# Kernel tuning notes

Measured on AMD Instinct MI355X. Metric: run time of the kernel, lower is better.

The kernel has to match this reference:

```python
import jax, jax.numpy as jnp
import numpy as np
from jax import lax

D_MODEL = 512
N_STATE = 64
L = 1024
NC = 4  # n_components
HIDDEN = 2 * D_MODEL  # ChannelMix mult=2
R = D_MODEL // 8      # SE reduction
EPS = 1e-5


def hippo_A(N):
    n = np.arange(N, dtype=np.float32)
    t = 2.0 * n + 1.0
    sq = np.sqrt(t[:, None] * t[None, :])
    A = -np.tril(sq, -1) - np.diag(n + 1.0)
    return jnp.asarray(A, jnp.float32)


def setup_inputs() -> dict:
    key = jax.random.key(0)
    ks = jax.random.split(key, 12)
    d, N = D_MODEL, N_STATE
    n = np.arange(N, dtype=np.float32)
    Bref = jnp.asarray(np.sqrt(2.0 * n + 1.0), jnp.float32)
    Bp = jnp.tile(Bref[None, None, :], (NC, d, 1)) + 0.01 * jax.random.normal(ks[0], (NC, d, N))
    Cp = 0.1 * jax.random.normal(ks[1], (NC, d, N))
    Dp = jnp.zeros((NC, d))
    log_dt = jnp.log(0.1 * (1.5 ** jnp.arange(NC, dtype=jnp.float32)))
    x = jax.random.normal(ks[2], (8, L, d))
    s = 0.02
    return {
        "x": x,
        "Bp": Bp, "Cp": Cp, "Dp": Dp, "log_dt": log_dt,
        "se_w1": s * jax.random.normal(ks[3], (R, d)), "se_b1": jnp.zeros((R,)),
        "se_w2": s * jax.random.normal(ks[4], (d, R)), "se_b2": jnp.zeros((d,)),
        "n1_g": jnp.ones((d,)), "n1_b": jnp.zeros((d,)),
        "up_w": s * jax.random.normal(ks[5], (2 * HIDDEN, d)), "up_b": jnp.zeros((2 * HIDDEN,)),
        "down_w": s * jax.random.normal(ks[6], (d, HIDDEN)), "down_b": jnp.zeros((d,)),
        "mixn_g": jnp.ones((d,)), "mixn_b": jnp.zeros((d,)),
        "n2_g": jnp.ones((d,)), "n2_b": jnp.zeros((d,)),
    }


def _ln(x, g, b):
    m = jnp.mean(x, axis=-1, keepdims=True)
    v = jnp.mean(jnp.square(x - m), axis=-1, keepdims=True)
    return (x - m) * lax.rsqrt(v + EPS) * g + b


def _mixture_kernel(Bp, Cp, Dp, log_dt):
    A = hippo_A(N_STATE)
    I = jnp.eye(N_STATE, dtype=jnp.float32)

    def one(Bc, Cc, Dc, ldt):
        dt = jax.nn.softplus(ldt) + 1e-6
        lhs = I - 0.5 * dt * A
        rhs = I + 0.5 * dt * A
        A_bar = jnp.linalg.solve(lhs, rhs)          # (N,N)
        B_bar = jnp.linalg.solve(lhs, (dt * Bc).T).T  # (d,N)

        def step(xs, _):
            y = jnp.einsum('dn,dn->d', Cc, xs)
            return xs @ A_bar.T, y

        _, ys = lax.scan(step, B_bar, None, length=L)  # (L,d)
        K = ys.T  # (d,L)
        return K.at[:, 0].add(Dc)

    return jax.vmap(one)(Bp, Cp, Dp, log_dt).sum(0)  # (d,L)


def reference(x, Bp, Cp, Dp, log_dt,
              se_w1, se_b1, se_w2, se_b2,
              n1_g, n1_b, up_w, up_b, down_w, down_b,
              mixn_g, mixn_b, n2_g, n2_b):
    d = D_MODEL
    K = _mixture_kernel(Bp, Cp, Dp, log_dt)  # (d,L)

    # causal full-length depthwise conv1d
    x_dw = jnp.transpose(x, (0, 2, 1))  # (B,C,T)
    x_pad = jnp.pad(x_dw, ((0, 0), (0, 0), (L - 1, 0)))
    y = lax.conv_general_dilated(
        x_pad, K[:, None, :], window_strides=(1,), padding='VALID',
        feature_group_count=d, dimension_numbers=('NCH', 'OIH', 'NCH'))
    y = jnp.transpose(y, (0, 2, 1))  # (B,T,C)

    # SE gate (squeeze over time)
    s = jnp.mean(y, axis=1)  # (B,C)
    h = jax.nn.relu(s @ se_w1.T + se_b1)
    g = jax.nn.sigmoid(h @ se_w2.T + se_b2)
    y = y * g[:, None, :]

    y1 = _ln(x + y, n1_g, n1_b)

    # ChannelMix (GLU MLP) with residual + LN
    u = y1 @ up_w.T + up_b
    a, gg = jnp.split(u, 2, axis=-1)
    z = (jax.nn.gelu(a, approximate=False) * jax.nn.sigmoid(gg)) @ down_w.T + down_b
    z = _ln(y1 + z, mixn_g, mixn_b)

    return _ln(y1 + z, n2_g, n2_b)
```

## Files before the change

kernel.cpp:

```cpp
#include <hip/hip_runtime.h>
#include <math.h>


typedef short bf16x8 __attribute__((ext_vector_type(8)));
typedef float f32x4 __attribute__((ext_vector_type(4)));

__device__ __forceinline__ float sigmoidf_(float x) { return 1.0f / (1.0f + expf(-x)); }
__device__ __forceinline__ float geluf_(float x) { return 0.5f * x * (1.0f + erff(x * 0.70710678118654752f)); }
__device__ __forceinline__ unsigned short f2bf(float f) {
    unsigned u = __float_as_uint(f);
    unsigned r = (u + 0x7FFFu + ((u >> 16) & 1u)) >> 16;
    return (unsigned short)r;
}
__device__ __forceinline__ unsigned pk2(unsigned short a, unsigned short b) {
    return (unsigned)a | ((unsigned)b << 16);
}

__global__ __launch_bounds__(256) void prep_comp(const float* __restrict__ log_dt,
                                                 float* __restrict__ Pow,
                                                 float* __restrict__ dtbuf) {
    int comp = blockIdx.x, tid = threadIdx.x;
    __shared__ __align__(16) float M1[4096];
    __shared__ __align__(16) float M1T[4096];
    __shared__ __align__(16) float M2[4096];
    __shared__ __align__(16) float M2T[4096];
    float ldt = log_dt[comp];
    float dt = log1pf(expf(ldt)) + 1e-6f;
    float hdt = 0.5f * dt;
    if (tid < 64) {
        int j = tid;
        float sqj = sqrtf(2.0f * (float)j + 1.0f);
        float S = 0.0f;
        for (int i = 0; i < 64; ++i) {
            float sqi = sqrtf(2.0f * (float)i + 1.0f);
            float r = (i == j) ? (1.0f - hdt * (float)(i + 1))
                               : ((i > j) ? (-hdt * sqi * sqj) : 0.0f);
            float X = (r - hdt * sqi * S) / (1.0f + hdt * (float)(i + 1));
            M1[i * 64 + j] = X;
            M1T[j * 64 + i] = X;
            S += sqi * X;
        }
    }
    __syncthreads();
    for (int ii = tid; ii < 4096; ii += 256) Pow[(size_t)comp * 40960 + ii] = M1[ii];
    float* cur = M1; float* curT = M1T; float* nxt = M2; float* nxtT = M2T;
    int ti = tid >> 4, tj = tid & 15;
    for (int s = 1; s <= 9; ++s) {
        float c[4][4] = {{0}};
#pragma unroll 8
        for (int k = 0; k < 64; ++k) {
            float4 a = *(const float4*)&curT[k * 64 + ti * 4];
            float4 b = *(const float4*)&cur[k * 64 + tj * 4];
            c[0][0] += a.x * b.x; c[0][1] += a.x * b.y; c[0][2] += a.x * b.z; c[0][3] += a.x * b.w;
            c[1][0] += a.y * b.x; c[1][1] += a.y * b.y; c[1][2] += a.y * b.z; c[1][3] += a.y * b.w;
            c[2][0] += a.z * b.x; c[2][1] += a.z * b.y; c[2][2] += a.z * b.z; c[2][3] += a.z * b.w;
            c[3][0] += a.w * b.x; c[3][1] += a.w * b.y; c[3][2] += a.w * b.z; c[3][3] += a.w * b.w;
        }
#pragma unroll
        for (int r = 0; r < 4; ++r) {
            float4 row; row.x = c[r][0]; row.y = c[r][1]; row.z = c[r][2]; row.w = c[r][3];
            *(float4*)&nxt[(ti * 4 + r) * 64 + tj * 4] = row;
            float4 colv; colv.x = c[0][r]; colv.y = c[1][r]; colv.z = c[2][r]; colv.w = c[3][r];
            *(float4*)&nxtT[(tj * 4 + r) * 64 + ti * 4] = colv;
        }
        __syncthreads();
        for (int ii = tid; ii < 4096; ii += 256) Pow[(size_t)comp * 40960 + s * 4096 + ii] = nxt[ii];
        float* t0 = cur; cur = nxt; nxt = t0;
        float* t1 = curT; curT = nxtT; nxtT = t1;
        __syncthreads();
    }
    if (tid == 0) dtbuf[comp] = dt;
}

__global__ __launch_bounds__(256) void compute_bbar(const float* __restrict__ Bp,
                                                    const float* __restrict__ dtbuf,
                                                    float* __restrict__ Bbar) {
    int gid = blockIdx.x * 256 + threadIdx.x;
    int comp = gid >> 9;
    float dt = dtbuf[comp];
    float hdt = 0.5f * dt;
    const float* bp = Bp + (size_t)gid * 64;
    float* out = Bbar + (size_t)gid * 64;
    float S = 0.0f;
    for (int i = 0; i < 64; ++i) {
        float sqi = sqrtf(2.0f * (float)i + 1.0f);
        float y = (dt * bp[i] - hdt * sqi * S) / (1.0f + hdt * (float)(i + 1));
        out[i] = y;
        S += sqi * y;
    }
}

__global__ __launch_bounds__(256) void f32_to_bf16_hl(const float* __restrict__ in,
                                                      unsigned short* __restrict__ oh,
                                                      unsigned short* __restrict__ ol,
                                                      int n8) {
    int i = blockIdx.x * 256 + threadIdx.x;
    if (i >= n8) return;
    float4 a = ((const float4*)in)[2 * i];
    float4 b = ((const float4*)in)[2 * i + 1];
    float vv[8] = {a.x, a.y, a.z, a.w, b.x, b.y, b.z, b.w};
    unsigned short hs[8], ls[8];
#pragma unroll
    for (int j = 0; j < 8; ++j) {
        unsigned short h = f2bf(vv[j]);
        hs[j] = h;
        ls[j] = f2bf(vv[j] - __uint_as_float((unsigned)h << 16));
    }
    uint4 ho, lo;
    ho.x = pk2(hs[0], hs[1]); ho.y = pk2(hs[2], hs[3]); ho.z = pk2(hs[4], hs[5]); ho.w = pk2(hs[6], hs[7]);
    lo.x = pk2(ls[0], ls[1]); lo.y = pk2(ls[2], ls[3]); lo.z = pk2(ls[4], ls[5]); lo.w = pk2(ls[6], ls[7]);
    *(uint4*)&oh[(size_t)i * 8] = ho;
    *(uint4*)&ol[(size_t)i * 8] = lo;
}

__global__ __launch_bounds__(256) void power_mats(const float* __restrict__ Pow,
                                                  unsigned short* __restrict__ Pst_h,
                                                  unsigned short* __restrict__ Pst_l,
                                                  unsigned short* __restrict__ Qst_h,
                                                  unsigned short* __restrict__ Qst_l) {
    int idx = blockIdx.x, comp = blockIdx.y, tid = threadIdx.x;
    __shared__ __align__(16) float R[4096], RT[4096], R2[4096], R2T[4096], SbT[4096];
    int isP = (idx < 32) ? 1 : 0;
    int f = isP ? idx : (idx - 32);
    int base_s = isP ? 0 : 5;
    const float* PowC = Pow + (size_t)comp * 40960;
    int i_ = tid & 63, kc = (tid >> 6) * 16;
    float* cur = R; float* curT = RT; float* nx = R2; float* nxT = R2T;
    if (f == 0) {
        for (int ii = tid; ii < 4096; ii += 256) {
            float v = ((ii >> 6) == (ii & 63)) ? 1.0f : 0.0f;
            R[ii] = v; RT[ii] = v;
        }
        __syncthreads();
    } else {
        int b0 = __ffs(f) - 1;
        const float* S0 = PowC + (size_t)(base_s + b0) * 4096;
#pragma unroll
        for (int j = 0; j < 16; j += 4) {
            float4 v = *(const float4*)&S0[i_ * 64 + kc + j];
            *(float4*)&R[i_ * 64 + kc + j] = v;
            RT[(kc + j + 0) * 64 + i_] = v.x;
            RT[(kc + j + 1) * 64 + i_] = v.y;
            RT[(kc + j + 2) * 64 + i_] = v.z;
            RT[(kc + j + 3) * 64 + i_] = v.w;
        }
        int rem = f & ~(1 << b0);
        int ti = tid >> 4, tj = tid & 15;
        __syncthreads();
        while (rem) {
            int b = __ffs(rem) - 1; rem &= rem - 1;
            const float* Sb = PowC + (size_t)(base_s + b) * 4096;
#pragma unroll
            for (int j = 0; j < 16; j += 4) {
                float4 v = *(const float4*)&Sb[i_ * 64 + kc + j];
                SbT[(kc + j + 0) * 64 + i_] = v.x;
                SbT[(kc + j + 1) * 64 + i_] = v.y;
                SbT[(kc + j + 2) * 64 + i_] = v.z;
                SbT[(kc + j + 3) * 64 + i_] = v.w;
            }
            __syncthreads();
            float c[4][4] = {{0}};
#pragma unroll 8
            for (int k = 0; k < 64; ++k) {
                float4 a = *(const float4*)&SbT[k * 64 + ti * 4];
                float4 b4 = *(const float4*)&cur[k * 64 + tj * 4];
                c[0][0] += a.x * b4.x; c[0][1] += a.x * b4.y; c[0][2] += a.x * b4.z; c[0][3] += a.x * b4.w;
                c[1][0] += a.y * b4.x; c[1][1] += a.y * b4.y; c[1][2] += a.y * b4.z; c[1][3] += a.y * b4.w;
                c[2][0] += a.z * b4.x; c[2][1] += a.z * b4.y; c[2][2] += a.z * b4.z; c[2][3] += a.z * b4.w;
                c[3][0] += a.w * b4.x; c[3][1] += a.w * b4.y; c[3][2] += a.w * b4.z; c[3][3] += a.w * b4.w;
            }
#pragma unroll
            for (int r = 0; r < 4; ++r) {
                float4 row; row.x = c[r][0]; row.y = c[r][1]; row.z = c[r][2]; row.w = c[r][3];
                *(float4*)&nx[(ti * 4 + r) * 64 + tj * 4] = row;
                float4 colv; colv.x = c[0][r]; colv.y = c[1][r]; colv.z = c[2][r]; colv.w = c[3][r];
                *(float4*)&nxT[(tj * 4 + r) * 64 + ti * 4] = colv;
            }
            __syncthreads();
            float* t0 = cur; cur = nx; nx = t0;
            float* t1 = curT; curT = nxT; nxT = t1;
        }
    }
    const float* src = isP ? cur : curT;
    int outrow = isP ? idx : (idx - 32);
    unsigned short* dh = (isP ? Pst_h : Qst_h) + (size_t)comp * 131072 + (size_t)outrow * 4096;
    unsigned short* dl = (isP ? Pst_l : Qst_l) + (size_t)comp * 131072 + (size_t)outrow * 4096;
    for (int ii = tid * 8; ii < 4096; ii += 2048) {
        float4 v0 = *(const float4*)&src[ii];
        float4 v1 = *(const float4*)&src[ii + 4];
        float vv[8] = {v0.x, v0.y, v0.z, v0.w, v1.x, v1.y, v1.z, v1.w};
        unsigned short hs[8], ls[8];
#pragma unroll
        for (int j = 0; j < 8; ++j) {
            unsigned short h = f2bf(vv[j]);
            hs[j] = h;
            ls[j] = f2bf(vv[j] - __uint_as_float((unsigned)h << 16));
        }
        uint4 ho, lo;
        ho.x = pk2(hs[0], hs[1]); ho.y = pk2(hs[2], hs[3]); ho.z = pk2(hs[4], hs[5]); ho.w = pk2(hs[6], hs[7]);
        lo.x = pk2(ls[0], ls[1]); lo.y = pk2(ls[2], ls[3]); lo.z = pk2(ls[4], ls[5]); lo.w = pk2(ls[6], ls[7]);
        *(uint4*)&dh[ii] = ho;
        *(uint4*)&dl[ii] = lo;
    }
}

__global__ __launch_bounds__(256) void kgemm_uv(const unsigned short* __restrict__ Ah,
                                                const unsigned short* __restrict__ Al,
                                                const unsigned short* __restrict__ Bh,
                                                const unsigned short* __restrict__ Bl,
                                                unsigned short* __restrict__ Ch,
                                                unsigned short* __restrict__ Cl) {
    int m0 = blockIdx.x * 128, n0 = blockIdx.y * 64, comp = blockIdx.z;
    int tid = threadIdx.x, w = tid >> 6, l = tid & 63;
    __shared__ __align__(16) short Ash[8192], Asl[8192], Bsh[4096], Bsl[4096];
    const unsigned short* Abh = Ah + (size_t)comp * 32768;
    const unsigned short* Abl = Al + (size_t)comp * 32768;
    const unsigned short* Bbh = Bh + (size_t)comp * 131072;
    const unsigned short* Bbl = Bl + (size_t)comp * 131072;
#pragma unroll
    for (int i = 0; i < 4; ++i) {
        int cid = tid + 256 * i;
        int row = cid >> 3, slot = cid & 7;
        int goff = (m0 + row) * 64 + slot * 8;
        int loff = row * 64 + (slot ^ (row & 7)) * 8;
        *(uint4*)&Ash[loff] = *(const uint4*)(Abh + goff);
        *(uint4*)&Asl[loff] = *(const uint4*)(Abl + goff);
    }
#pragma unroll
    for (int i = 0; i < 2; ++i) {
        int cid = tid + 256 * i;
        int row = cid >> 3, slot = cid & 7;
        int goff = (n0 + row) * 64 + slot * 8;
        int loff = row * 64 + (slot ^ (row & 7)) * 8;
        *(uint4*)&Bsh[loff] = *(const uint4*)(Bbh + goff);
        *(uint4*)&Bsl[loff] = *(const uint4*)(Bbl + goff);
    }
    __syncthreads();
    int p = l >> 4, lr = l & 15;
    f32x4 acc[2][4];
#pragma unroll
    for (int rt = 0; rt < 2; ++rt)
#pragma unroll
        for (int ct = 0; ct < 4; ++ct) acc[rt][ct] = (f32x4)0.0f;
#pragma unroll
    for (int ks = 0; ks < 2; ++ks) {
        bf16x8 ah2[2], al2[2], bh2[4], bl2[4];
#pragma unroll
        for (int rt = 0; rt < 2; ++rt) {
            int row = w * 32 + rt * 16 + lr;
            int off = row * 64 + ((ks * 4 + p) ^ (row & 7)) * 8;
            ah2[rt] = *(bf16x8*)&Ash[off];
            al2[rt] = *(bf16x8*)&Asl[off];
        }
#pragma unroll
        for (int ct = 0; ct < 4; ++ct) {
            int cr = ct * 16 + lr;
            int off = cr * 64 + ((ks * 4 + p) ^ (cr & 7)) * 8;
            bh2[ct] = *(bf16x8*)&Bsh[off];
            bl2[ct] = *(bf16x8*)&Bsl[off];
        }
#pragma unroll
        for (int rt = 0; rt < 2; ++rt)
#pragma unroll
            for (int ct = 0; ct < 4; ++ct) {
                acc[rt][ct] = __builtin_amdgcn_mfma_f32_16x16x32_bf16(ah2[rt], bh2[ct], acc[rt][ct], 0, 0, 0);
                acc[rt][ct] = __builtin_amdgcn_mfma_f32_16x16x32_bf16(ah2[rt], bl2[ct], acc[rt][ct], 0, 0, 0);
                acc[rt][ct] = __builtin_amdgcn_mfma_f32_16x16x32_bf16(al2[rt], bh2[ct], acc[rt][ct], 0, 0, 0);
            }
    }
#pragma unroll
    for (int rt = 0; rt < 2; ++rt)
#pragma unroll
        for (int ct = 0; ct < 4; ++ct) {
#pragma unroll
            for (int reg = 0; reg < 4; ++reg) {
                int row = m0 + w * 32 + rt * 16 + p * 4 + reg;
                int col = n0 + ct * 16 + lr;
                float v = acc[rt][ct][reg];
                unsigned short h = f2bf(v);
                unsigned short lo2 = f2bf(v - __uint_as_float((unsigned)h << 16));
                size_t o = (size_t)comp * 1048576 + (size_t)row * 2048 + col;
                Ch[o] = h;
                Cl[o] = lo2;
            }
        }
}

__global__ __launch_bounds__(256) void kgemm_k(const unsigned short* __restrict__ Uh,
                                               const unsigned short* __restrict__ Ul,
                                               const unsigned short* __restrict__ Vh,
                                               const unsigned short* __restrict__ Vl,
                                               float* __restrict__ Kpart) {
    int tid = threadIdx.x, w = tid >> 6, l = tid & 63;
    int g = blockIdx.x * 4 + w;
    int p = l >> 4, lr = l & 15;
    const unsigned short* ubh = Uh + (size_t)g * 2048;
    const unsigned short* ubl = Ul + (size_t)g * 2048;
    const unsigned short* vbh = Vh + (size_t)g * 2048;
    const unsigned short* vbl = Vl + (size_t)g * 2048;
    f32x4 acc[2][2];
    acc[0][0] = (f32x4)0.0f; acc[0][1] = (f32x4)0.0f;
    acc[1][0] = (f32x4)0.0f; acc[1][1] = (f32x4)0.0f;
#pragma unroll
    for (int ks = 0; ks < 2; ++ks) {
        bf16x8 uh2[2], ul2[2], vh2[2], vl2[2];
#pragma unroll
        for (int mt = 0; mt < 2; ++mt) {
            int off = (mt * 16 + lr) * 64 + ks * 32 + p * 8;
            uh2[mt] = *(const bf16x8*)(ubh + off);
            ul2[mt] = *(const bf16x8*)(ubl + off);
            vh2[mt] = *(const bf16x8*)(vbh + off);
            vl2[mt] = *(const bf16x8*)(vbl + off);
        }
#pragma unroll
        for (int mt = 0; mt < 2; ++mt)
#pragma unroll
            for (int nt = 0; nt < 2; ++nt) {
                acc[mt][nt] = __builtin_amdgcn_mfma_f32_16x16x32_bf16(uh2[mt], vh2[nt], acc[mt][nt], 0, 0, 0);
                acc[mt][nt] = __builtin_amdgcn_mfma_f32_16x16x32_bf16(uh2[mt], vl2[nt], acc[mt][nt], 0, 0, 0);
                acc[mt][nt] = __builtin_amdgcn_mfma_f32_16x16x32_bf16(ul2[mt], vh2[nt], acc[mt][nt], 0, 0, 0);
            }
    }
#pragma unroll
    for (int mt = 0; mt < 2; ++mt)
#pragma unroll
        for (int nt = 0; nt < 2; ++nt)
#pragma unroll
            for (int reg = 0; reg < 4; ++reg) {
                int q = mt * 16 + p * 4 + reg;
                int r = nt * 16 + lr;
                Kpart[(size_t)g * 1024 + q * 32 + r] = acc[mt][nt][reg];
            }
}

__global__ __launch_bounds__(256) void reduce_K(const float* __restrict__ Kpart,
                                                const float* __restrict__ Dp,
                                                float* __restrict__ Kr) {
    int idx = blockIdx.x * 256 + threadIdx.x;
    int d = idx >> 10, l = idx & 1023;
    float s = Kpart[idx] + Kpart[524288 + idx] + Kpart[1048576 + idx] + Kpart[1572864 + idx];
    if (l == 0) s += Dp[d] + Dp[512 + d] + Dp[1024 + d] + Dp[1536 + d];
    Kr[(size_t)d * 1024 + (1023 - l)] = s;
}

__global__ __launch_bounds__(256) void transpose_bmat(const float* __restrict__ in,
                                                      float* __restrict__ out,
                                                      int R, int C) {
    __shared__ float tile[32][33];
    int r0 = blockIdx.x * 32, c0 = blockIdx.y * 32, b = blockIdx.z;
    int tx = threadIdx.x & 31, ty = threadIdx.x >> 5;
#pragma unroll
    for (int m = 0; m < 4; ++m)
        tile[ty + 8 * m][tx] = in[((size_t)b * R + r0 + ty + 8 * m) * C + c0 + tx];
    __syncthreads();
#pragma unroll
    for (int m = 0; m < 4; ++m)
        out[((size_t)b * C + c0 + ty + 8 * m) * R + r0 + tx] = tile[tx][ty + 8 * m];
}

__global__ __launch_bounds__(256) void conv_mfma(const float* __restrict__ xT,
                                                 const float* __restrict__ Kr,
                                                 float* __restrict__ yT,
                                                 float* __restrict__ ssum) {
    int c = blockIdx.x, tid = threadIdx.x;
    int w = tid >> 6, l = tid & 63;
    __shared__ __align__(16) float krp[1088];
    __shared__ __align__(16) short xh[8512], xl[8512];
    __shared__ __align__(16) short gh[10240], gl[10240];
    __shared__ float ssh[64];

    {
        float4 kv = *(const float4*)&Kr[(size_t)c * 1024 + tid * 4];
        *(float4*)&krp[32 + tid * 4] = kv;
        if (tid < 8) *(float4*)&krp[tid * 4] = make_float4(0, 0, 0, 0);
        else if (tid < 16) *(float4*)&krp[1056 + (tid - 8) * 4] = make_float4(0, 0, 0, 0);
    }
    if (tid < 32) {
        int b = tid >> 2, g = tid & 3;
        uint4 z = {0, 0, 0, 0};
        *(uint4*)&xh[(b * 133 + g) * 8] = z;
    } else if (tid < 64) {
        int t2 = tid - 32; int b = t2 >> 2, g = t2 & 3;
        uint4 z = {0, 0, 0, 0};
        *(uint4*)&xl[(b * 133 + g) * 8] = z;
    }
#pragma unroll
    for (int i = 0; i < 4; ++i) {
        int gid = tid + 256 * i;
        int b = gid >> 7, gt = gid & 127;
        const float* src = &xT[((size_t)(b * 512 + c)) * 1024 + gt * 8];
        float4 v0 = *(const float4*)src;
        float4 v1 = *(const float4*)(src + 4);
        float vv[8] = {v0.x, v0.y, v0.z, v0.w, v1.x, v1.y, v1.z, v1.w};
        unsigned short hsv[8], lsv[8];
#pragma unroll
        for (int j2 = 0; j2 < 8; ++j2) {
            unsigned short h = f2bf(vv[j2]);
            hsv[j2] = h;
            lsv[j2] = f2bf(vv[j2] - __uint_as_float((unsigned)h << 16));
        }
        uint4 hh, ll;
        hh.x = pk2(hsv[0], hsv[1]); hh.y = pk2(hsv[2], hsv[3]);
        hh.z = pk2(hsv[4], hsv[5]); hh.w = pk2(hsv[6], hsv[7]);
        ll.x = pk2(lsv[0], lsv[1]); ll.y = pk2(lsv[2], lsv[3]);
        ll.z = pk2(lsv[4], lsv[5]); ll.w = pk2(lsv[6], lsv[7]);
        int off = (b * 133 + 4 + gt) * 8;
        *(uint4*)&xh[off] = hh;
        *(uint4*)&xl[off] = ll;
    }
    __syncthreads();

    f32x4 acc[4][2];
#pragma unroll
    for (int i = 0; i < 4; ++i) { acc[i][0] = (f32x4)0.0f; acc[i][1] = (f32x4)0.0f; }

    int lr = l & 15, kg4 = l >> 4;
    for (int ch = 0; ch < 4; ++ch) {
        int dq0 = ch * 8;
        {
            int dqloc = tid >> 5, n = tid & 31, dq = dq0 + dqloc;
            int s0 = 32 * dq + n + 1;
            int a0 = s0 & ~3, sh = s0 & 3;
            float ff[36];
#pragma unroll
            for (int i = 0; i < 9; ++i) *(float4*)&ff[i * 4] = *(const float4*)&krp[a0 + i * 4];
// ... 74 lines not shown
    for (int off = 1; off < 16; off <<= 1) {
#pragma unroll
        for (int reg = 0; reg < 4; ++reg) bsum[reg] += __shfl_xor(bsum[reg], off, 64);
    }
    if (lr == 0) {
#pragma unroll
        for (int reg = 0; reg < 4; ++reg) ssh[w * 16 + kg4 * 4 + reg] = bsum[reg];
    }
    __syncthreads();
    if (tid < 8) {
        float tot = 0.0f;
        for (int w2 = 0; w2 < 4; ++w2) tot += ssh[w2 * 16 + tid] + ssh[w2 * 16 + 8 + tid];
        ssum[tid * 512 + c] = tot;
    }
}

__global__ __launch_bounds__(256) void se_kernel(const float* __restrict__ ssum,
                                                 const float* __restrict__ w1,
                                                 const float* __restrict__ b1,
                                                 const float* __restrict__ w2,
                                                 const float* __restrict__ b2,
                                                 float* __restrict__ g) {
    int b = blockIdx.x, tid = threadIdx.x;
    __shared__ float s_sh[512];
    __shared__ float part[256];
    __shared__ float h_sh[64];
    for (int c = tid; c < 512; c += 256) s_sh[c] = ssum[b * 512 + c] * (1.0f / 1024.0f);
    __syncthreads();
    int r = tid & 63, seg = tid >> 6;
    float p = 0.0f;
    for (int c = seg * 128; c < seg * 128 + 128; ++c) p += s_sh[c] * w1[r * 512 + c];
    part[tid] = p;
    __syncthreads();
    if (tid < 64) {
        float h = part[tid] + part[tid + 64] + part[tid + 128] + part[tid + 192] + b1[tid];
        h_sh[tid] = fmaxf(h, 0.0f);
    }
    __syncthreads();
    for (int c = tid; c < 512; c += 256) {
        float acc = b2[c];
#pragma unroll 8
        for (int rr = 0; rr < 64; ++rr) acc += h_sh[rr] * w2[c * 64 + rr];
        g[b * 512 + c] = 1.0f / (1.0f + expf(-acc));
    }
}

__global__ __launch_bounds__(128) void fuse1_kernel(const float* __restrict__ x,
                                                    const float* __restrict__ y,
                                                    const float* __restrict__ g,
                                                    const float* __restrict__ n1g,
                                                    const float* __restrict__ n1b,
                                                    unsigned short* __restrict__ y1b) {
    int row = blockIdx.x, b = row >> 10, tid = threadIdx.x, c = tid * 4;
    __shared__ float r1[2], r2[2];
    float4 xv = *(const float4*)&x[(size_t)row * 512 + c];
    float4 yv = *(const float4*)&y[(size_t)row * 512 + c];
    float4 gv = *(const float4*)&g[b * 512 + c];
    float4 v;
    v.x = xv.x + yv.x * gv.x; v.y = xv.y + yv.y * gv.y;
    v.z = xv.z + yv.z * gv.z; v.w = xv.w + yv.w * gv.w;
    float s1 = v.x + v.y + v.z + v.w;
    float s2 = v.x * v.x + v.y * v.y + v.z * v.z + v.w * v.w;
#pragma unroll
    for (int off = 32; off > 0; off >>= 1) {
        s1 += __shfl_down(s1, off, 64);
        s2 += __shfl_down(s2, off, 64);
    }
    if ((tid & 63) == 0) { r1[tid >> 6] = s1; r2[tid >> 6] = s2; }
    __syncthreads();
    float mean = (r1[0] + r1[1]) * (1.0f / 512.0f);
    float var = (r2[0] + r2[1]) * (1.0f / 512.0f) - mean * mean;
    float rstd = rsqrtf(var + 1e-5f);
    float4 g4 = *(const float4*)&n1g[c];
    float4 b4 = *(const float4*)&n1b[c];
    float4 o;
    o.x = (v.x - mean) * rstd * g4.x + b4.x; o.y = (v.y - mean) * rstd * g4.y + b4.y;
    o.z = (v.z - mean) * rstd * g4.z + b4.z; o.w = (v.w - mean) * rstd * g4.w + b4.w;
    uint2 pk;
    pk.x = pk2(f2bf(o.x), f2bf(o.y));
    pk.y = pk2(f2bf(o.z), f2bf(o.w));
    *(uint2*)&y1b[(size_t)row * 512 + c] = pk;
}

__global__ __launch_bounds__(256) void f32_to_bf16(const float* __restrict__ in,
                                                   unsigned short* __restrict__ out,
                                                   int n8) {
    int i = blockIdx.x * 256 + threadIdx.x;
    if (i >= n8) return;
    float4 a = ((const float4*)in)[2 * i];
    float4 b = ((const float4*)in)[2 * i + 1];
    uint4 o;
    o.x = pk2(f2bf(a.x), f2bf(a.y));
    o.y = pk2(f2bf(a.z), f2bf(a.w));
    o.z = pk2(f2bf(b.x), f2bf(b.y));
    o.w = pk2(f2bf(b.z), f2bf(b.w));
    *(uint4*)&out[(size_t)i * 8] = o;
}

__device__ __forceinline__ int swz_slot(int slot, int row) {
    return slot ^ (row & 3) ^ ((row >> 2) & 3);
}

__global__ __launch_bounds__(256) void gemm_glu(const unsigned short* __restrict__ A,
                                                const unsigned short* __restrict__ W,
                                                const float* __restrict__ bias,
                                                unsigned short* __restrict__ act) {
    const int K = 512;
    int m0 = blockIdx.x * 128, n0 = blockIdx.y * 64;
    int tid = threadIdx.x, w = tid >> 6, l = tid & 63;
    __shared__ short As[4096];
    __shared__ short Bs[4096];
    int idA0 = tid, idA1 = tid + 256;
    int rA0 = idA0 >> 2, sA0 = idA0 & 3, rA1 = idA1 >> 2, sA1 = idA1 & 3;
    int ldsA0 = rA0 * 32 + swz_slot(sA0, rA0) * 8;
    int ldsA1 = rA1 * 32 + swz_slot(sA1, rA1) * 8;
    const unsigned short* pA0 = A + (size_t)(m0 + rA0) * K + sA0 * 8;
    const unsigned short* pA1 = A + (size_t)(m0 + rA1) * K + sA1 * 8;
    int gB0 = (rA0 < 64) ? (n0 + rA0) : (1024 + n0 + rA0 - 64);
    int gB1 = (rA1 < 64) ? (n0 + rA1) : (1024 + n0 + rA1 - 64);
    const unsigned short* pB0 = W + (size_t)gB0 * K + sA0 * 8;
    const unsigned short* pB1 = W + (size_t)gB1 * K + sA1 * 8;
    int p = l >> 4, lr = l & 15;
    int aoff[2], bAoff[4], bGoff[4];
#pragma unroll
    for (int rt = 0; rt < 2; ++rt) {
        int r = w * 32 + rt * 16 + lr;
        aoff[rt] = r * 32 + swz_slot(p, r) * 8;
    }
#pragma unroll
    for (int ct = 0; ct < 4; ++ct) {
        int ca = ct * 16 + lr, cg = 64 + ct * 16 + lr;
        bAoff[ct] = ca * 32 + swz_slot(p, ca) * 8;
        bGoff[ct] = cg * 32 + swz_slot(p, cg) * 8;
    }
    f32x4 accA[2][4], accG[2][4];
#pragma unroll
    for (int rt = 0; rt < 2; ++rt)
#pragma unroll
        for (int ct = 0; ct < 4; ++ct) {
            accA[rt][ct] = (f32x4)0.0f;
            accG[rt][ct] = (f32x4)0.0f;
        }
    for (int kt = 0; kt < K; kt += 32) {
        uint4 va0 = *(const uint4*)pA0;
        uint4 va1 = *(const uint4*)pA1;
        uint4 vb0 = *(const uint4*)pB0;
        uint4 vb1 = *(const uint4*)pB1;
        __syncthreads();
        *(uint4*)&As[ldsA0] = va0;
        *(uint4*)&As[ldsA1] = va1;
        *(uint4*)&Bs[ldsA0] = vb0;
        *(uint4*)&Bs[ldsA1] = vb1;
        __syncthreads();
        bf16x8 af[2], bA[4], bG[4];
#pragma unroll
        for (int rt = 0; rt < 2; ++rt) af[rt] = *(bf16x8*)&As[aoff[rt]];
#pragma unroll
        for (int ct = 0; ct < 4; ++ct) {
            bA[ct] = *(bf16x8*)&Bs[bAoff[ct]];
            bG[ct] = *(bf16x8*)&Bs[bGoff[ct]];
        }
#pragma unroll
        for (int rt = 0; rt < 2; ++rt)
#pragma unroll
            for (int ct = 0; ct < 4; ++ct) {
                accA[rt][ct] = __builtin_amdgcn_mfma_f32_16x16x32_bf16(af[rt], bA[ct], accA[rt][ct], 0, 0, 0);
                accG[rt][ct] = __builtin_amdgcn_mfma_f32_16x16x32_bf16(af[rt], bG[ct], accG[rt][ct], 0, 0, 0);
            }
        pA0 += 32; pA1 += 32; pB0 += 32; pB1 += 32;
    }
#pragma unroll
    for (int rt = 0; rt < 2; ++rt)
#pragma unroll
        for (int ct = 0; ct < 4; ++ct) {
            int col = n0 + ct * 16 + lr;
            float ba = bias[col], bg = bias[1024 + col];
#pragma unroll
            for (int reg = 0; reg < 4; ++reg) {
                int row = m0 + w * 32 + rt * 16 + p * 4 + reg;
                float a = accA[rt][ct][reg] + ba;
                float g = accG[rt][ct][reg] + bg;
                act[(size_t)row * 1024 + col] = f2bf(geluf_(a) * sigmoidf_(g));
            }
        }
}

__global__ __launch_bounds__(256) void gemm_plain(const unsigned short* __restrict__ A,
                                                  const unsigned short* __restrict__ W,
                                                  const float* __restrict__ bias,
                                                  float* __restrict__ Cout) {
    const int K = 1024, N = 512;
    int m0 = blockIdx.x * 128, n0 = blockIdx.y * 128;
    int tid = threadIdx.x, w = tid >> 6, l = tid & 63;
    int wr = w >> 1, wc = w & 1;
    __shared__ short As[4096];
    __shared__ short Bs[4096];
    int idA0 = tid, idA1 = tid + 256;
    int rA0 = idA0 >> 2, sA0 = idA0 & 3, rA1 = idA1 >> 2, sA1 = idA1 & 3;
    int ldsA0 = rA0 * 32 + swz_slot(sA0, rA0) * 8;
    int ldsA1 = rA1 * 32 + swz_slot(sA1, rA1) * 8;
    const unsigned short* pA0 = A + (size_t)(m0 + rA0) * K + sA0 * 8;
    const unsigned short* pA1 = A + (size_t)(m0 + rA1) * K + sA1 * 8;
    const unsigned short* pB0 = W + (size_t)(n0 + rA0) * K + sA0 * 8;
    const unsigned short* pB1 = W + (size_t)(n0 + rA1) * K + sA1 * 8;
    int p = l >> 4, lr = l & 15;
    int aoff[4], boff[4];
#pragma unroll
    for (int t = 0; t < 4; ++t) {
        int r = wr * 64 + t * 16 + lr;
        aoff[t] = r * 32 + swz_slot(p, r) * 8;
        int cq = wc * 64 + t * 16 + lr;
        boff[t] = cq * 32 + swz_slot(p, cq) * 8;
    }
    f32x4 acc[4][4];
#pragma unroll
    for (int i = 0; i < 4; ++i)
#pragma unroll
        for (int j = 0; j < 4; ++j) acc[i][j] = (f32x4)0.0f;
    for (int kt = 0; kt < K; kt += 32) {
        uint4 va0 = *(const uint4*)pA0;
        uint4 va1 = *(const uint4*)pA1;
        uint4 vb0 = *(const uint4*)pB0;
        uint4 vb1 = *(const uint4*)pB1;
        __syncthreads();
        *(uint4*)&As[ldsA0] = va0;
        *(uint4*)&As[ldsA1] = va1;
        *(uint4*)&Bs[ldsA0] = vb0;
        *(uint4*)&Bs[ldsA1] = vb1;
        __syncthreads();
        bf16x8 af[4], bfr[4];
#pragma unroll
        for (int t = 0; t < 4; ++t) {
            af[t] = *(bf16x8*)&As[aoff[t]];
            bfr[t] = *(bf16x8*)&Bs[boff[t]];
        }
#pragma unroll
        for (int i = 0; i < 4; ++i)
#pragma unroll
            for (int j = 0; j < 4; ++j)
                acc[i][j] = __builtin_amdgcn_mfma_f32_16x16x32_bf16(af[i], bfr[j], acc[i][j], 0, 0, 0);
        pA0 += 32; pA1 += 32; pB0 += 32; pB1 += 32;
    }
#pragma unroll
    for (int i = 0; i < 4; ++i)
#pragma unroll
        for (int j = 0; j < 4; ++j) {
            int col = n0 + wc * 64 + j * 16 + lr;
            float bb = bias[col];
#pragma unroll
            for (int reg = 0; reg < 4; ++reg) {
                int row = m0 + wr * 64 + i * 16 + p * 4 + reg;
                Cout[(size_t)row * N + col] = acc[i][j][reg] + bb;
            }
        }
}

__global__ __launch_bounds__(128) void fuse2_kernel(const unsigned short* __restrict__ y1b,
                                                    const float* __restrict__ z,
                                                    const float* __restrict__ mg,
                                                    const float* __restrict__ mb,
                                                    const float* __restrict__ g2,
                                                    const float* __restrict__ b2v,
                                                    float* __restrict__ out) {
    int row = blockIdx.x, tid = threadIdx.x, c = tid * 4;
    __shared__ float r1[2], r2[2];
    uint2 yu = *(const uint2*)&y1b[(size_t)row * 512 + c];
    float4 a;
    a.x = __uint_as_float(yu.x << 16);
    a.y = __uint_as_float(yu.x & 0xffff0000u);
    a.z = __uint_as_float(yu.y << 16);
    a.w = __uint_as_float(yu.y & 0xffff0000u);
    float4 zv = *(const float4*)&z[(size_t)row * 512 + c];
    float4 t1;
    t1.x = a.x + zv.x; t1.y = a.y + zv.y; t1.z = a.z + zv.z; t1.w = a.w + zv.w;
    float s1 = t1.x + t1.y + t1.z + t1.w;
    float s2 = t1.x * t1.x + t1.y * t1.y + t1.z * t1.z + t1.w * t1.w;
#pragma unroll
    for (int off = 32; off > 0; off >>= 1) {
        s1 += __shfl_down(s1, off, 64);
        s2 += __shfl_down(s2, off, 64);
    }
    if ((tid & 63) == 0) { r1[tid >> 6] = s1; r2[tid >> 6] = s2; }
    __syncthreads();
    float mean = (r1[0] + r1[1]) * (1.0f / 512.0f);
    float var = (r2[0] + r2[1]) * (1.0f / 512.0f) - mean * mean;
    float rstd = rsqrtf(var + 1e-5f);
    float4 mg4 = *(const float4*)&mg[c];
    float4 mb4 = *(const float4*)&mb[c];
    float4 t2;
    t2.x = a.x + ((t1.x - mean) * rstd * mg4.x + mb4.x);
    t2.y = a.y + ((t1.y - mean) * rstd * mg4.y + mb4.y);
    t2.z = a.z + ((t1.z - mean) * rstd * mg4.z + mb4.z);
    t2.w = a.w + ((t1.w - mean) * rstd * mg4.w + mb4.w);
    __syncthreads();
    s1 = t2.x + t2.y + t2.z + t2.w;
    s2 = t2.x * t2.x + t2.y * t2.y + t2.z * t2.z + t2.w * t2.w;
#pragma unroll
    for (int off = 32; off > 0; off >>= 1) {
        s1 += __shfl_down(s1, off, 64);
        s2 += __shfl_down(s2, off, 64);
    }
    if ((tid & 63) == 0) { r1[tid >> 6] = s1; r2[tid >> 6] = s2; }
    __syncthreads();
    float mean2 = (r1[0] + r1[1]) * (1.0f / 512.0f);
    float var2 = (r2[0] + r2[1]) * (1.0f / 512.0f) - mean2 * mean2;
    float rstd2 = rsqrtf(var2 + 1e-5f);
    float4 gg = *(const float4*)&g2[c];
    float4 bb = *(const float4*)&b2v[c];
    float4 o;
    o.x = (t2.x - mean2) * rstd2 * gg.x + bb.x;
    o.y = (t2.y - mean2) * rstd2 * gg.y + bb.y;
    o.z = (t2.z - mean2) * rstd2 * gg.z + bb.z;
    o.w = (t2.w - mean2) * rstd2 * gg.w + bb.w;
    *(float4*)&out[(size_t)row * 512 + c] = o;
}

extern "C" void kernel_launch(void* const* d_in, const int* in_sizes, int n_in,
                              void* d_out, int out_size, void* d_ws, size_t ws_size,
                              hipStream_t stream) {
    (void)in_sizes; (void)n_in; (void)out_size; (void)ws_size;
    const float* x      = (const float*)d_in[0];
    const float* Bp     = (const float*)d_in[1];
    const float* Cp     = (const float*)d_in[2];
    const float* Dp     = (const float*)d_in[3];
    const float* log_dt = (const float*)d_in[4];
    const float* se_w1  = (const float*)d_in[5];
    const float* se_b1  = (const float*)d_in[6];
    const float* se_w2  = (const float*)d_in[7];
    const float* se_b2  = (const float*)d_in[8];
    const float* n1g    = (const float*)d_in[9];
    const float* n1b    = (const float*)d_in[10];
    const float* up_w   = (const float*)d_in[11];
    const float* up_b   = (const float*)d_in[12];
    const float* dn_w   = (const float*)d_in[13];
    const float* dn_b   = (const float*)d_in[14];
    const float* mxg    = (const float*)d_in[15];
    const float* mxb    = (const float*)d_in[16];
    const float* n2g    = (const float*)d_in[17];
    const float* n2b    = (const float*)d_in[18];

    float* ws = (float*)d_ws;
    float* Kr   = ws + 0;
    float* dtb  = ws + 524288;
    float* ssum = ws + 524352;
    float* gbuf = ws + 528448;
    unsigned short* up_wb = (unsigned short*)(ws + 532544);
    unsigned short* dn_wb = (unsigned short*)(ws + 1056832);
    float* Bbar = ws + 1318976;
    float* Pow  = ws + 1450048;
    unsigned short* Bb_h = (unsigned short*)(ws + 1613888);
    unsigned short* Bb_l = (unsigned short*)(ws + 1679424);
    unsigned short* Cp_h = (unsigned short*)(ws + 1744960);
    unsigned short* Cp_l = (unsigned short*)(ws + 1810496);
    unsigned short* Pst_h = (unsigned short*)(ws + 1876032);
    unsigned short* Pst_l = (unsigned short*)(ws + 2138176);
    unsigned short* Qst_h = (unsigned short*)(ws + 2400320);
    unsigned short* Qst_l = (unsigned short*)(ws + 2662464);
    float* Kpart = ws + 2924608;
    unsigned short* U_h = (unsigned short*)(ws + 5021760);
    unsigned short* U_l = (unsigned short*)(ws + 7118912);
    unsigned short* V_h = (unsigned short*)(ws + 9216064);
    unsigned short* V_l = (unsigned short*)(ws + 11313216);
    float* xT   = ws + 5021760;
    float* yT   = ws + 9216064;
    float* yb   = ws + 13410368;
    unsigned short* y1b = (unsigned short*)(ws + 9216064);
    unsigned short* act = (unsigned short*)(ws + 5021760);
    float* zb   = ws + 13410368;
    float* outp = (float*)d_out;

    hipLaunchKernelGGL(prep_comp, dim3(4), dim3(256), 0, stream, log_dt, Pow, dtb);
    hipLaunchKernelGGL(compute_bbar, dim3(8), dim3(256), 0, stream, Bp, dtb, Bbar);
    hipLaunchKernelGGL(f32_to_bf16_hl, dim3(64), dim3(256), 0, stream, Bbar, Bb_h, Bb_l, 16384);
    hipLaunchKernelGGL(f32_to_bf16_hl, dim3(64), dim3(256), 0, stream, Cp, Cp_h, Cp_l, 16384);
    hipLaunchKernelGGL(power_mats, dim3(64, 4), dim3(256), 0, stream, Pow, Pst_h, Pst_l, Qst_h, Qst_l);
    hipLaunchKernelGGL(kgemm_uv, dim3(4, 32, 4), dim3(256), 0, stream, Bb_h, Bb_l, Pst_h, Pst_l, V_h, V_l);
    hipLaunchKernelGGL(kgemm_uv, dim3(4, 32, 4), dim3(256), 0, stream, Cp_h, Cp_l, Qst_h, Qst_l, U_h, U_l);
    hipLaunchKernelGGL(kgemm_k, dim3(512), dim3(256), 0, stream, U_h, U_l, V_h, V_l, Kpart);
    hipLaunchKernelGGL(reduce_K, dim3(2048), dim3(256), 0, stream, Kpart, Dp, Kr);
    hipLaunchKernelGGL(f32_to_bf16, dim3(512), dim3(256), 0, stream, up_w, up_wb, 131072);
    hipLaunchKernelGGL(f32_to_bf16, dim3(256), dim3(256), 0, stream, dn_w, dn_wb, 65536);
    hipLaunchKernelGGL(transpose_bmat, dim3(32, 16, 8), dim3(256), 0, stream, x, xT, 1024, 512);
    hipLaunchKernelGGL(conv_mfma, dim3(512), dim3(256), 0, stream, xT, Kr, yT, ssum);
    hipLaunchKernelGGL(se_kernel, dim3(8), dim3(256), 0, stream, ssum, se_w1, se_b1, se_w2, se_b2, gbuf);
    hipLaunchKernelGGL(transpose_bmat, dim3(16, 32, 8), dim3(256), 0, stream, yT, yb, 512, 1024);
    hipLaunchKernelGGL(fuse1_kernel, dim3(8192), dim3(128), 0, stream, x, yb, gbuf, n1g, n1b, y1b);
    hipLaunchKernelGGL(gemm_glu, dim3(64, 16), dim3(256), 0, stream, y1b, up_wb, up_b, act);
    hipLaunchKernelGGL(gemm_plain, dim3(64, 4), dim3(256), 0, stream, act, dn_wb, dn_b, zb);
    hipLaunchKernelGGL(fuse2_kernel, dim3(8192), dim3(128), 0, stream, y1b, zb, mxg, mxb, n2g, n2b, outp);
}
```

Measured before the change: 240.2 us.

## Fuse setup kernels, fold K reduction into GEMM, use direct global-to-LDS loads

Several small setup kernels are merged: B_bar is converted to hi/lo bf16 inside compute_bbar, all weight and Cp conversions run in one launch, and the two U/V GEMMs share one grid. The K partial-sum reduction and Dp add move into the K GEMM through shared memory, which removes the Kpart round trip and a launch. The GLU and plain GEMMs now load tiles with global_load_lds straight into LDS instead of going through registers. This cuts launch count and global traffic, but changes how K-GEMM work is mapped to blocks and depends on correct LDS layout for the async loads.

```diff
diff --git a/kernel.cpp b/kernel.cpp
--- a/kernel.cpp
+++ b/kernel.cpp
@@ -14,6 +14,10 @@
 }
 __device__ __forceinline__ unsigned pk2(unsigned short a, unsigned short b) {
     return (unsigned)a | ((unsigned)b << 16);
+}
+__device__ __forceinline__ void gload16(const void* g, void* l) {
+    __builtin_amdgcn_global_load_lds((const __attribute__((address_space(1))) unsigned int*)g,
+                                     (__attribute__((address_space(3))) unsigned int*)l, 16, 0, 0);
 }
 
 __global__ __launch_bounds__(256) void prep_comp(const float* __restrict__ log_dt,
@@ -74,43 +78,64 @@
 
 __global__ __launch_bounds__(256) void compute_bbar(const float* __restrict__ Bp,
                                                     const float* __restrict__ dtbuf,
-                                                    float* __restrict__ Bbar) {
+                                                    unsigned short* __restrict__ Bb_h,
+                                                    unsigned short* __restrict__ Bb_l) {
     int gid = blockIdx.x * 256 + threadIdx.x;
     int comp = gid >> 9;
     float dt = dtbuf[comp];
     float hdt = 0.5f * dt;
     const float* bp = Bp + (size_t)gid * 64;
-    float* out = Bbar + (size_t)gid * 64;
+    unsigned short* oh = Bb_h + (size_t)gid * 64;
+    unsigned short* ol = Bb_l + (size_t)gid * 64;
     float S = 0.0f;
     for (int i = 0; i < 64; ++i) {
         float sqi = sqrtf(2.0f * (float)i + 1.0f);
         float y = (dt * bp[i] - hdt * sqi * S) / (1.0f + hdt * (float)(i + 1));
-        out[i] = y;
+        unsigned short h = f2bf(y);
+        oh[i] = h;
+        ol[i] = f2bf(y - __uint_as_float((unsigned)h << 16));
         S += sqi * y;
     }
 }
 
-__global__ __launch_bounds__(256) void f32_to_bf16_hl(const float* __restrict__ in,
-                                                      unsigned short* __restrict__ oh,
-                                                      unsigned short* __restrict__ ol,
-                                                      int n8) {
+__global__ __launch_bounds__(256) void convert_all(const float* __restrict__ up_w,
+                                                   const float* __restrict__ dn_w,
+                                                   const float* __restrict__ Cp,
+                                                   unsigned short* __restrict__ up_wb,
+                                                   unsigned short* __restrict__ dn_wb,
+                                                   unsigned short* __restrict__ Cp_h,
+                                                   unsigned short* __restrict__ Cp_l) {
     int i = blockIdx.x * 256 + threadIdx.x;
-    if (i >= n8) return;
-    float4 a = ((const float4*)in)[2 * i];
-    float4 b = ((const float4*)in)[2 * i + 1];
-    float vv[8] = {a.x, a.y, a.z, a.w, b.x, b.y, b.z, b.w};
-    unsigned short hs[8], ls[8];
-#pragma unroll
-    for (int j = 0; j < 8; ++j) {
-        unsigned short h = f2bf(vv[j]);
-        hs[j] = h;
-        ls[j] = f2bf(vv[j] - __uint_as_float((unsigned)h << 16));
-    }
-    uint4 ho, lo;
-    ho.x = pk2(hs[0], hs[1]); ho.y = pk2(hs[2], hs[3]); ho.z = pk2(hs[4], hs[5]); ho.w = pk2(hs[6], hs[7]);
-    lo.x = pk2(ls[0], ls[1]); lo.y = pk2(ls[2], ls[3]); lo.z = pk2(ls[4], ls[5]); lo.w = pk2(ls[6], ls[7]);
-    *(uint4*)&oh[(size_t)i * 8] = ho;
-    *(uint4*)&ol[(size_t)i * 8] = lo;
+    if (i < 196608) {
+        const float* src = (i < 131072) ? up_w : dn_w;
+        unsigned short* dst = (i < 131072) ? up_wb : dn_wb;
+        int j = (i < 131072) ? i : (i - 131072);
+        float4 a = ((const float4*)src)[2 * j];
+        float4 b = ((const float4*)src)[2 * j + 1];
+        uint4 o;
+        o.x = pk2(f2bf(a.x), f2bf(a.y));
+        o.y = pk2(f2bf(a.z), f2bf(a.w));
+        o.z = pk2(f2bf(b.x), f2bf(b.y));
+        o.w = pk2(f2bf(b.z), f2bf(b.w));
+        *(uint4*)&dst[(size_t)j * 8] = o;
+    } else if (i < 212992) {
+        int j = i - 196608;
+        float4 a = ((const float4*)Cp)[2 * j];
+        float4 b = ((const float4*)Cp)[2 * j + 1];
+        float vv[8] = {a.x, a.y, a.z, a.w, b.x, b.y, b.z, b.w};
+        unsigned short hs[8], ls[8];
+#pragma unroll
+        for (int k = 0; k < 8; ++k) {
+            unsigned short h = f2bf(vv[k]);
+            hs[k] = h;
+            ls[k] = f2bf(vv[k] - __uint_as_float((unsigned)h << 16));
+        }
+        uint4 ho, lo;
+        ho.x = pk2(hs[0], hs[1]); ho.y = pk2(hs[2], hs[3]); ho.z = pk2(hs[4], hs[5]); ho.w = pk2(hs[6], hs[7]);
+        lo.x = pk2(ls[0], ls[1]); lo.y = pk2(ls[2], ls[3]); lo.z = pk2(ls[4], ls[5]); lo.w = pk2(ls[6], ls[7]);
+        *(uint4*)&Cp_h[(size_t)j * 8] = ho;
+        *(uint4*)&Cp_l[(size_t)j * 8] = lo;
+    }
 }
 
 __global__ __launch_bounds__(256) void power_mats(const float* __restrict__ Pow,
@@ -204,13 +229,28 @@
     }
 }
 
-__global__ __launch_bounds__(256) void kgemm_uv(const unsigned short* __restrict__ Ah,
-                                                const unsigned short* __restrict__ Al,
-                                                const unsigned short* __restrict__ Bh,
-                                                const unsigned short* __restrict__ Bl,
-                                                unsigned short* __restrict__ Ch,
-                                                unsigned short* __restrict__ Cl) {
-    int m0 = blockIdx.x * 128, n0 = blockIdx.y * 64, comp = blockIdx.z;
+__global__ __launch_bounds__(256) void kgemm_uv2(const unsigned short* __restrict__ Bb_h,
+                                                 const unsigned short* __restrict__ Bb_l,
+                                                 const unsigned short* __restrict__ Pst_h,
+                                                 const unsigned short* __restrict__ Pst_l,
+                                                 const unsigned short* __restrict__ Cp_h,
+                                                 const unsigned short* __restrict__ Cp_l,
+                                                 const unsigned short* __restrict__ Qst_h,
+                                                 const unsigned short* __restrict__ Qst_l,
+                                                 unsigned short* __restrict__ V_h,
+                                                 unsigned short* __restrict__ V_l,
+                                                 unsigned short* __restrict__ U_h,
+                                                 unsigned short* __restrict__ U_l) {
+    int zz = blockIdx.z;
+    int isV = (zz < 4) ? 1 : 0;
+    int comp = isV ? zz : (zz - 4);
+    const unsigned short* Ah = isV ? Bb_h : Cp_h;
+    const unsigned short* Al = isV ? Bb_l : Cp_l;
+    const unsigned short* Bh = isV ? Pst_h : Qst_h;
+    const unsigned short* Bl = isV ? Pst_l : Qst_l;
+    unsigned short* Ch = isV ? V_h : U_h;
+    unsigned short* Cl = isV ? V_l : U_l;
+    int m0 = blockIdx.x * 128, n0 = blockIdx.y * 64;
     int tid = threadIdx.x, w = tid >> 6, l = tid & 63;
     __shared__ __align__(16) short Ash[8192], Asl[8192], Bsh[4096], Bsl[4096];
     const unsigned short* Abh = Ah + (size_t)comp * 32768;
@@ -286,14 +326,17 @@
         }
 }
 
-__global__ __launch_bounds__(256) void kgemm_k(const unsigned short* __restrict__ Uh,
-                                               const unsigned short* __restrict__ Ul,
-                                               const unsigned short* __restrict__ Vh,
-                                               const unsigned short* __restrict__ Vl,
-                                               float* __restrict__ Kpart) {
+__global__ __launch_bounds__(256) void kgemm_kr(const unsigned short* __restrict__ Uh,
+                                                const unsigned short* __restrict__ Ul,
+                                                const unsigned short* __restrict__ Vh,
+                                                const unsigned short* __restrict__ Vl,
+                                                const float* __restrict__ Dp,
+                                                float* __restrict__ Kr) {
     int tid = threadIdx.x, w = tid >> 6, l = tid & 63;
-    int g = blockIdx.x * 4 + w;
+    int d = blockIdx.x;
+    int g = w * 512 + d;
     int p = l >> 4, lr = l & 15;
+    __shared__ float ksh[4096];
     const unsigned short* ubh = Uh + (size_t)g * 2048;
     const unsigned short* ubl = Ul + (size_t)g * 2048;
     const unsigned short* vbh = Vh + (size_t)g * 2048;
@@ -329,18 +372,16 @@
             for (int reg = 0; reg < 4; ++reg) {
                 int q = mt * 16 + p * 4 + reg;
                 int r = nt * 16 + lr;
-                Kpart[(size_t)g * 1024 + q * 32 + r] = acc[mt][nt][reg];
-            }
-}
-
-__global__ __launch_bounds__(256) void reduce_K(const float* __restrict__ Kpart,
-                                                const float* __restrict__ Dp,
-                                                float* __restrict__ Kr) {
-    int idx = blockIdx.x * 256 + threadIdx.x;
-    int d = idx >> 10, l = idx & 1023;
-    float s = Kpart[idx] + Kpart[524288 + idx] + Kpart[1048576 + idx] + Kpart[1572864 + idx];
-    if (l == 0) s += Dp[d] + Dp[512 + d] + Dp[1024 + d] + Dp[1536 + d];
-    Kr[(size_t)d * 1024 + (1023 - l)] = s;
+                ksh[w * 1024 + q * 32 + r] = acc[mt][nt][reg];
+            }
+    __syncthreads();
+#pragma unroll
+    for (int j = 0; j < 4; ++j) {
+        int ll = tid * 4 + j;
+        float s = ksh[ll] + ksh[1024 + ll] + ksh[2048 + ll] + ksh[3072 + ll];
+        if (ll == 0) s += Dp[d] + Dp[512 + d] + Dp[1024 + d] + Dp[1536 + d];
+        Kr[(size_t)d * 1024 + (1023 - ll)] = s;
+    }
 }
 
 __global__ __launch_bounds__(256) void transpose_bmat(const float* __restrict__ in,
@@ -581,21 +622,6 @@
     *(uint2*)&y1b[(size_t)row * 512 + c] = pk;
 }
 
-__global__ __launch_bounds__(256) void f32_to_bf16(const float* __restrict__ in,
-                                                   unsigned short* __restrict__ out,
-                                                   int n8) {
-    int i = blockIdx.x * 256 + threadIdx.x;
-    if (i >= n8) return;
-    float4 a = ((const float4*)in)[2 * i];
-    float4 b = ((const float4*)in)[2 * i + 1];
-    uint4 o;
-    o.x = pk2(f2bf(a.x), f2bf(a.y));
-    o.y = pk2(f2bf(a.z), f2bf(a.w));
-    o.z = pk2(f2bf(b.x), f2bf(b.y));
-    o.w = pk2(f2bf(b.z), f2bf(b.w));
-    *(uint4*)&out[(size_t)i * 8] = o;
-}
-
 __device__ __forceinline__ int swz_slot(int slot, int row) {
     return slot ^ (row & 3) ^ ((row >> 2) & 3);
 }
@@ -607,18 +633,22 @@
     const int K = 512;
     int m0 = blockIdx.x * 128, n0 = blockIdx.y * 64;
     int tid = threadIdx.x, w = tid >> 6, l = tid & 63;
-    __shared__ short As[4096];
-    __shared__ short Bs[4096];
-    int idA0 = tid, idA1 = tid + 256;
-    int rA0 = idA0 >> 2, sA0 = idA0 & 3, rA1 = idA1 >> 2, sA1 = idA1 & 3;
-    int ldsA0 = rA0 * 32 + swz_slot(sA0, rA0) * 8;
-    int ldsA1 = rA1 * 32 + swz_slot(sA1, rA1) * 8;
-    const unsigned short* pA0 = A + (size_t)(m0 + rA0) * K + sA0 * 8;
-    const unsigned short* pA1 = A + (size_t)(m0 + rA1) * K + sA1 * 8;
-    int gB0 = (rA0 < 64) ? (n0 + rA0) : (1024 + n0 + rA0 - 64);
-    int gB1 = (rA1 < 64) ? (n0 + rA1) : (1024 + n0 + rA1 - 64);
-    const unsigned short* pB0 = W + (size_t)gB0 * K + sA0 * 8;
-    const unsigned short* pB1 = W + (size_t)gB1 * K + sA1 * 8;
+    __shared__ __align__(16) short As[4096];
+    __shared__ __align__(16) short Bs[4096];
+    int seg0 = 2 * w, seg1 = 2 * w + 1;
+    int rA0 = seg0 * 16 + (l >> 2), rA1 = seg1 * 16 + (l >> 2);
+    int ss0 = (l & 3) ^ (rA0 & 3) ^ ((rA0 >> 2) & 3);
+    int ss1 = (l & 3) ^ (rA1 & 3) ^ ((rA1 >> 2) & 3);
+    const unsigned short* gA0 = A + (size_t)(m0 + rA0) * K + ss0 * 8;
+    const unsigned short* gA1 = A + (size_t)(m0 + rA1) * K + ss1 * 8;
+    int gBr0 = (rA0 < 64) ? (n0 + rA0) : (1024 + n0 + rA0 - 64);
+    int gBr1 = (rA1 < 64) ? (n0 + rA1) : (1024 + n0 + rA1 - 64);
+    const unsigned short* gB0 = W + (size_t)gBr0 * K + ss0 * 8;
+    const unsigned short* gB1 = W + (size_t)gBr1 * K + ss1 * 8;
+    short* ldsA0 = &As[seg0 * 512];
+    short* ldsA1 = &As[seg1 * 512];
+    short* ldsB0 = &Bs[seg0 * 512];
+    short* ldsB1 = &Bs[seg1 * 512];
     int p = l >> 4, lr = l & 15;
     int aoff[2], bAoff[4], bGoff[4];
 #pragma unroll
@@ -641,15 +671,11 @@
             accG[rt][ct] = (f32x4)0.0f;
         }
     for (int kt = 0; kt < K; kt += 32) {
-        uint4 va0 = *(const uint4*)pA0;
-        uint4 va1 = *(const uint4*)pA1;
-        uint4 vb0 = *(const uint4*)pB0;
-        uint4 vb1 = *(const uint4*)pB1;
         __syncthreads();
-        *(uint4*)&As[ldsA0] = va0;
-        *(uint4*)&As[ldsA1] = va1;
-        *(uint4*)&Bs[ldsA0] = vb0;
-        *(uint4*)&Bs[ldsA1] = vb1;
+        gload16(gA0 + kt, ldsA0);
+        gload16(gA1 + kt, ldsA1);
+        gload16(gB0 + kt, ldsB0);
+        gload16(gB1 + kt, ldsB1);
         __syncthreads();
         bf16x8 af[2], bA[4], bG[4];
 #pragma unroll
@@ -666,7 +692,6 @@
                 accA[rt][ct] = __builtin_amdgcn_mfma_f32_16x16x32_bf16(af[rt], bA[ct], accA[rt][ct], 0, 0, 0);
                 accG[rt][ct] = __builtin_amdgcn_mfma_f32_16x16x32_bf16(af[rt], bG[ct], accG[rt][ct], 0, 0, 0);
             }
-        pA0 += 32; pA1 += 32; pB0 += 32; pB1 += 32;
     }
 #pragma unroll
     for (int rt = 0; rt < 2; ++rt)
@@ -692,16 +717,20 @@
     int m0 = blockIdx.x * 128, n0 = blockIdx.y * 128;
     int tid = threadIdx.x, w = tid >> 6, l = tid & 63;
     int wr = w >> 1, wc = w & 1;
-    __shared__ short As[4096];
-    __shared__ short Bs[4096];
-    int idA0 = tid, idA1 = tid + 256;
-    int rA0 = idA0 >> 2, sA0 = idA0 & 3, rA1 = idA1 >> 2, sA1 = idA1 & 3;
-    int ldsA0 = rA0 * 32 + swz_slot(sA0, rA0) * 8;
-    int ldsA1 = rA1 * 32 + swz_slot(sA1, rA1) * 8;
-    const unsigned short* pA0 = A + (size_t)(m0 + rA0) * K + sA0 * 8;
-    const unsigned short* pA1 = A + (size_t)(m0 + rA1) * K + sA1 * 8;
-    const unsigned short* pB0 = W + (size_t)(n0 + rA0) * K + sA0 * 8;
-    const unsigned short* pB1 = W + (size_t)(n0 + rA1) * K + sA1 * 8;
+    __shared__ __align__(16) short As[4096];
+    __shared__ __align__(16) short Bs[4096];
+    int seg0 = 2 * w, seg1 = 2 * w + 1;
+    int rA0 = seg0 * 16 + (l >> 2), rA1 = seg1 * 16 + (l >> 2);
+    int ss0 = (l & 3) ^ (rA0 & 3) ^ ((rA0 >> 2) & 3);
+    int ss1 = (l & 3) ^ (rA1 & 3) ^ ((rA1 >> 2) & 3);
+    const unsigned short* gA0 = A + (size_t)(m0 + rA0) * K + ss0 * 8;
+    const unsigned short* gA1 = A + (size_t)(m0 + rA1) * K + ss1 * 8;
+    const unsigned short* gB0 = W + (size_t)(n0 + rA0) * K + ss0 * 8;
+    const unsigned short* gB1 = W + (size_t)(n0 + rA1) * K + ss1 * 8;
+    short* ldsA0 = &As[seg0 * 512];
+    short* ldsA1 = &As[seg1 * 512];
+    short* ldsB0 = &Bs[seg0 * 512];
+    short* ldsB1 = &Bs[seg1 * 512];
     int p = l >> 4, lr = l & 15;
     int aoff[4], boff[4];
 #pragma unroll
@@ -717,15 +746,11 @@
 #pragma unroll
         for (int j = 0; j < 4; ++j) acc[i][j] = (f32x4)0.0f;
     for (int kt = 0; kt < K; kt += 32) {
-        uint4 va0 = *(const uint4*)pA0;
-        uint4 va1 = *(const uint4*)pA1;
-        uint4 vb0 = *(const uint4*)pB0;
-        uint4 vb1 = *(const uint4*)pB1;
         __syncthreads();
-        *(uint4*)&As[ldsA0] = va0;
-        *(uint4*)&As[ldsA1] = va1;
-        *(uint4*)&Bs[ldsA0] = vb0;
-        *(uint4*)&Bs[ldsA1] = vb1;
+        gload16(gA0 + kt, ldsA0);
+        gload16(gA1 + kt, ldsA1);
+        gload16(gB0 + kt, ldsB0);
+        gload16(gB1 + kt, ldsB1);
         __syncthreads();
         bf16x8 af[4], bfr[4];
 #pragma unroll
@@ -738,7 +763,6 @@
 #pragma unroll
             for (int j = 0; j < 4; ++j)
                 acc[i][j] = __builtin_amdgcn_mfma_f32_16x16x32_bf16(af[i], bfr[j], acc[i][j], 0, 0, 0);
-        pA0 += 32; pA1 += 32; pB0 += 32; pB1 += 32;
     }
 #pragma unroll
     for (int i = 0; i < 4; ++i)
@@ -845,7 +869,6 @@
     float* gbuf = ws + 528448;
     unsigned short* up_wb = (unsigned short*)(ws + 532544);
     unsigned short* dn_wb = (unsigned short*)(ws + 1056832);
-    float* Bbar = ws + 1318976;
     float* Pow  = ws + 1450048;
     unsigned short* Bb_h = (unsigned short*)(ws + 1613888);
     unsigned short* Bb_l = (unsigned short*)(ws + 1679424);
@@ -855,7 +878,6 @@
     unsigned short* Pst_l = (unsigned short*)(ws + 2138176);
     unsigned short* Qst_h = (unsigned short*)(ws + 2400320);
     unsigned short* Qst_l = (unsigned short*)(ws + 2662464);
-    float* Kpart = ws + 2924608;
     unsigned short* U_h = (unsigned short*)(ws + 5021760);
     unsigned short* U_l = (unsigned short*)(ws + 7118912);
     unsigned short* V_h = (unsigned short*)(ws + 9216064);
@@ -869,16 +891,12 @@
     float* outp = (float*)d_out;
 
     hipLaunchKernelGGL(prep_comp, dim3(4), dim3(256), 0, stream, log_dt, Pow, dtb);
-    hipLaunchKernelGGL(compute_bbar, dim3(8), dim3(256), 0, stream, Bp, dtb, Bbar);
-    hipLaunchKernelGGL(f32_to_bf16_hl, dim3(64), dim3(256), 0, stream, Bbar, Bb_h, Bb_l, 16384);
-    hipLaunchKernelGGL(f32_to_bf16_hl, dim3(64), dim3(256), 0, stream, Cp, Cp_h, Cp_l, 16384);
+    hipLaunchKernelGGL(compute_bbar, dim3(8), dim3(256), 0, stream, Bp, dtb, Bb_h, Bb_l);
+    hipLaunchKernelGGL(convert_all, dim3(832), dim3(256), 0, stream, up_w, dn_w, Cp, up_wb, dn_wb, Cp_h, Cp_l);
     hipLaunchKernelGGL(power_mats, dim3(64, 4), dim3(256), 0, stream, Pow, Pst_h, Pst_l, Qst_h, Qst_l);
-    hipLaunchKernelGGL(kgemm_uv, dim3(4, 32, 4), dim3(256), 0, stream, Bb_h, Bb_l, Pst_h, Pst_l, V_h, V_l);
-    hipLaunchKernelGGL(kgemm_uv, dim3(4, 32, 4), dim3(256), 0, stream, Cp_h, Cp_l, Qst_h, Qst_l, U_h, U_l);
-    hipLaunchKernelGGL(kgemm_k, dim3(512), dim3(256), 0, stream, U_h, U_l, V_h, V_l, Kpart);
-    hipLaunchKernelGGL(reduce_K, dim3(2048), dim3(256), 0, stream, Kpart, Dp, Kr);
-    hipLaunchKernelGGL(f32_to_bf16, dim3(512), dim3(256), 0, stream, up_w, up_wb, 131072);
-    hipLaunchKernelGGL(f32_to_bf16, dim3(256), dim3(256), 0, stream, dn_w, dn_wb, 65536);
+    hipLaunchKernelGGL(kgemm_uv2, dim3(4, 32, 8), dim3(256), 0, stream,
+                       Bb_h, Bb_l, Pst_h, Pst_l, Cp_h, Cp_l, Qst_h, Qst_l, V_h, V_l, U_h, U_l);
+    hipLaunchKernelGGL(kgemm_kr, dim3(512), dim3(256), 0, stream, U_h, U_l, V_h, V_l, Dp, Kr);
     hipLaunchKernelGGL(transpose_bmat, dim3(32, 16, 8), dim3(256), 0, stream, x, xT, 1024, 512);
     hipLaunchKernelGGL(conv_mfma, dim3(512), dim3(256), 0, stream, xT, Kr, yT, ssum);
     hipLaunchKernelGGL(se_kernel, dim3(8), dim3(256), 0, stream, ssum, se_w1, se_b1, se_w2, se_b2, gbuf);
```

After: 235.1 us. 2.1% less time.
